# Performance work log

Measured on AMD Instinct MI355X. Metric: run time of the kernel, lower is better.

## Reference

```python
import jax, jax.numpy as jnp
import numpy as np

N_NODES = 100000
N_EDGES = 1600000
D = 128
EPS = 0.0  # train_eps=False -> constant


def setup_inputs() -> dict:
    key = jax.random.key(0)
    k = jax.random.split(key, 6)
    s = 1.0 / np.sqrt(D)
    return {
        "X": jax.random.normal(k[0], (N_NODES, D), dtype=jnp.float32),
        "W1": jax.random.normal(k[1], (D, D), dtype=jnp.float32) * s,
        "b1": jnp.zeros((D,), dtype=jnp.float32),
        "W2": jax.random.normal(k[2], (D, D), dtype=jnp.float32) * s,
        "b2": jnp.zeros((D,), dtype=jnp.float32),
        "edge_src": jax.random.randint(k[3], (N_EDGES,), 0, N_NODES, dtype=jnp.int32),
        "edge_dst": jax.random.randint(k[4], (N_EDGES,), 0, N_NODES, dtype=jnp.int32),
    }


def reference(X, W1, b1, W2, b2, edge_src, edge_dst):
    # v2v sum aggregation: agg[i] = sum_{j in N(i)} X[j]
    msgs = X[edge_src]  # (E, D) gather
    agg = jax.ops.segment_sum(msgs, edge_dst, num_segments=N_NODES)  # (N, D)
    h = (1.0 + EPS) * X + agg
    # MLP: Linear -> ReLU -> Linear
    h = jax.nn.relu(h @ W1 + b1)
    out = h @ W2 + b2
    return out
```

## Files before the change

### kernel.cpp

```cpp
#include <hip/hip_runtime.h>
#include <hip/hip_bf16.h>

#define N_NODES 100000
#define N_EDGES 1600000
#define D 128

#define NBINS 196
#define BINSHIFT 9
#define BINCAP 10000
#define EPB 8192

#define PREP_BIN_BLOCKS 196
#define PREP_W_BLOCKS 8
#define PREP_CVT_BLOCKS 3125

typedef __bf16 bf16x8 __attribute__((ext_vector_type(8)));
typedef short short8 __attribute__((ext_vector_type(8)));
typedef float f32x4 __attribute__((ext_vector_type(4)));

__device__ __forceinline__ unsigned short f2bf(float f) {
  union { float f; unsigned u; } c; c.f = f;
  unsigned u = c.u;
  u += 0x7FFFu + ((u >> 16) & 1u);
  return (unsigned short)(u >> 16);
}
__device__ __forceinline__ float bflo(unsigned u) {
  union { unsigned u; float f; } c; c.u = u << 16; return c.f;
}
__device__ __forceinline__ float bfhi(unsigned u) {
  union { unsigned u; float f; } c; c.u = u & 0xFFFF0000u; return c.f;
}

#define PADK 136

__launch_bounds__(512)
__global__ void k_prep(const float* __restrict__ X, unsigned short* __restrict__ Xb,
                       const float* __restrict__ W1, const float* __restrict__ W2,
                       unsigned short* __restrict__ Wimg,
                       const int* __restrict__ esrc, const int* __restrict__ edst,
                       int* __restrict__ g_bincnt, unsigned* __restrict__ binbuf) {
  __shared__ int cnt[NBINS];
  __shared__ int base[NBINS];
  const int b = blockIdx.x, t = threadIdx.x;

  if (b < PREP_BIN_BLOCKS) {
    const int e0 = b * EPB;
    const int ne = min(EPB, N_EDGES - e0);
    for (int i = t; i < NBINS; i += 512) cnt[i] = 0;
    __syncthreads();
    for (int i = t; i < ne; i += 512)
      atomicAdd(&cnt[edst[e0 + i] >> BINSHIFT], 1);
    __syncthreads();
    for (int i = t; i < NBINS; i += 512) {
      base[i] = atomicAdd(&g_bincnt[i], cnt[i]);
      cnt[i] = 0;
    }
    __syncthreads();
    for (int i = t; i < ne; i += 512) {
      int d = edst[e0 + i];
      int s = esrc[e0 + i];
      int bi = d >> BINSHIFT;
      int pos = base[bi] + atomicAdd(&cnt[bi], 1);
      binbuf[(size_t)bi * BINCAP + pos] = ((unsigned)(d & 511) << 17) | (unsigned)s;
    }
    return;
  }
  if (b < PREP_BIN_BLOCKS + PREP_W_BLOCKS) {
    int bb = b - PREP_BIN_BLOCKS;
    const float* W = (bb & 4) ? W2 : W1;
    unsigned short* img = Wimg + ((bb & 4) ? 128 * PADK : 0);
    int k0 = (bb & 3) * 32;
#pragma unroll
    for (int it = 0; it < 8; ++it) {
      int idx = it * 512 + t;
      int k = k0 + (idx >> 7), n = idx & 127;
      img[n * PADK + k] = f2bf(W[k * 128 + n]);
    }
    return;
  }
  size_t i = ((size_t)(b - PREP_BIN_BLOCKS - PREP_W_BLOCKS) * 512 + t) * 8;
  const float4* p = (const float4*)(X + i);
  float4 a = p[0], c = p[1];
  short8 s;
  s[0] = f2bf(a.x); s[1] = f2bf(a.y); s[2] = f2bf(a.z); s[3] = f2bf(a.w);
  s[4] = f2bf(c.x); s[5] = f2bf(c.y); s[6] = f2bf(c.z); s[7] = f2bf(c.w);
  *(short8*)(Xb + i) = s;
}

__launch_bounds__(512)
__global__ void k_binsort(const unsigned* __restrict__ binbuf, const int* __restrict__ g_bincnt,
                          int* __restrict__ srt, int* __restrict__ deg,
                          int* __restrict__ offs) {
  __shared__ int hist[512];
  __shared__ int scan[512];
  __shared__ int sb[256];
  const int b = blockIdx.x, t = threadIdx.x;

  if (t < 256) sb[t] = (t < NBINS) ? g_bincnt[t] : 0;
  __syncthreads();
  for (int d = 1; d < 256; d <<= 1) {
    int x = 0;
    if (t < 256 && t >= d) x = sb[t - d];
    __syncthreads();
    if (t < 256) sb[t] += x;
    __syncthreads();
  }
  const int cntb = g_bincnt[b];
  const int gbase = (b == 0) ? 0 : sb[b - 1];
  const int n0 = b << BINSHIFT;
  const unsigned* ebuf = binbuf + (size_t)b * BINCAP;

  hist[t] = 0;
  __syncthreads();
  for (int i = t; i < cntb; i += 512)
    atomicAdd(&hist[ebuf[i] >> 17], 1);
  __syncthreads();
  int v = hist[t];
  scan[t] = v;
  __syncthreads();
  for (int d = 1; d < 512; d <<= 1) {
    int x = (t >= d) ? scan[t - d] : 0;
    __syncthreads();
    scan[t] += x;
    __syncthreads();
  }
  int n = n0 + t;
  if (n < N_NODES) {
    deg[n] = v;
    offs[n] = gbase + scan[t] - v;
  }
  hist[t] = scan[t] - v;
  __syncthreads();
  for (int i = t; i < cntb; i += 512) {
    unsigned e = ebuf[i];
    int pos = atomicAdd(&hist[e >> 17], 1);
    srt[gbase + pos] = (int)(e & 0x1FFFFu);
  }
}


__global__ void k_hist(const int* __restrict__ dst, int* __restrict__ deg) {
  int i = blockIdx.x * 256 + threadIdx.x;
  if (i < N_EDGES) atomicAdd(&deg[dst[i]], 1);
}

__global__ void k_scan1(const int* __restrict__ deg, int* __restrict__ offs,
                        int* __restrict__ bsum) {
  __shared__ int s[1024];
  int t = threadIdx.x;
  int i = blockIdx.x * 1024 + t;
  int v = (i < N_NODES) ? deg[i] : 0;
  s[t] = v;
  __syncthreads();
  for (int d = 1; d < 1024; d <<= 1) {
    int x = (t >= d) ? s[t - d] : 0;
    __syncthreads();
    s[t] += x;
    __syncthreads();
  }
  if (i < N_NODES) offs[i] = s[t] - v;
  if (t == 1023) bsum[blockIdx.x] = s[t];
}

__global__ void k_scan2(int* __restrict__ bsum) {
  __shared__ int s[128];
  int t = threadIdx.x;
  int v = (t < 98) ? bsum[t] : 0;
  s[t] = v;
  __syncthreads();
  for (int d = 1; d < 128; d <<= 1) {
    int x = (t >= d) ? s[t - d] : 0;
    __syncthreads();
    s[t] += x;
    __syncthreads();
  }
  if (t < 98) bsum[t] = s[t] - v;
}

__global__ void k_scan3(int* __restrict__ offs, const int* __restrict__ bsum) {
  int i = blockIdx.x * 1024 + threadIdx.x;
  if (i < N_NODES) offs[i] += bsum[blockIdx.x];
}

__global__ void k_bucket(const int* __restrict__ src, const int* __restrict__ dst,
                         int* __restrict__ offs, int* __restrict__ srt) {
  int i = blockIdx.x * 256 + threadIdx.x;
  if (i < N_EDGES) {
    int pos = atomicAdd(&offs[dst[i]], 1);
    srt[pos] = src[i];
  }
}

__global__ void k_gather_bf(const unsigned int* __restrict__ X1,
                            const int* __restrict__ deg, const int* __restrict__ offs,
                            const int* __restrict__ srt, unsigned int* __restrict__ h0) {
  int node = blockIdx.x * 4 + (threadIdx.x >> 6);
  int lane = threadIdx.x & 63;
  unsigned u = X1[(size_t)node * 64 + lane];
  float hx = bflo(u), hy = bfhi(u);
  int e = offs[node];
  int end = e + deg[node];
  for (; e + 8 <= end; e += 8) {
    int s0 = srt[e],     s1 = srt[e + 1], s2 = srt[e + 2], s3 = srt[e + 3];
    int s4 = srt[e + 4], s5 = srt[e + 5], s6 = srt[e + 6], s7 = srt[e + 7];
    unsigned u0 = X1[(size_t)s0 * 64 + lane];
    unsigned u1 = X1[(size_t)s1 * 64 + lane];
    unsigned u2 = X1[(size_t)s2 * 64 + lane];
    unsigned u3 = X1[(size_t)s3 * 64 + lane];
    unsigned u4 = X1[(size_t)s4 * 64 + lane];
    unsigned u5 = X1[(size_t)s5 * 64 + lane];
    unsigned u6 = X1[(size_t)s6 * 64 + lane];
    unsigned u7 = X1[(size_t)s7 * 64 + lane];
    hx += bflo(u0); hy += bfhi(u0);
    hx += bflo(u1); hy += bfhi(u1);
    hx += bflo(u2); hy += bfhi(u2);
    hx += bflo(u3); hy += bfhi(u3);
    hx += bflo(u4); hy += bfhi(u4);
    hx += bflo(u5); hy += bfhi(u5);
    hx += bflo(u6); hy += bfhi(u6);
    hx += bflo(u7); hy += bfhi(u7);
  }
  for (; e + 2 <= end; e += 2) {
    unsigned u0 = X1[(size_t)srt[e] * 64 + lane];
    unsigned u1 = X1[(size_t)srt[e + 1] * 64 + lane];
    hx += bflo(u0); hy += bfhi(u0);
    hx += bflo(u1); hy += bfhi(u1);
  }
  for (; e < end; ++e) {
    unsigned u0 = X1[(size_t)srt[e] * 64 + lane];
    hx += bflo(u0); hy += bfhi(u0);
  }
  h0[(size_t)node * 64 + lane] = ((unsigned)f2bf(hy) << 16) | f2bf(hx);
}

__global__ void k_gather(const float* __restrict__ X, const int* __restrict__ deg,
                         const int* __restrict__ offs, const int* __restrict__ srt,
                         float* __restrict__ out) {
  int node = blockIdx.x * 4 + (threadIdx.x >> 6);
  int lane = threadIdx.x & 63;
  const float2* X2 = (const float2*)X;
  float2 h = X2[(size_t)node * 64 + lane];
  int end = offs[node];
  int dg = deg[node];
  for (int e = end - dg; e < end; ++e) {
    int s = srt[e];
    float2 x = X2[(size_t)s * 64 + lane];
    h.x += x.x; h.y += x.y;
  }
  ((float2*)out)[(size_t)node * 64 + lane] = h;
}

#define BR 256

template <bool BF>
__launch_bounds__(512, 1)
__global__ void k_mlp(const void* __restrict__ h0v,
                      const float* __restrict__ W1, const float* __restrict__ b1,
                      const float* __restrict__ W2, const float* __restrict__ b2,
                      const unsigned short* __restrict__ Wimg,
                      float* __restrict__ out) {
  __shared__ __attribute__((aligned(16))) unsigned short lW[2 * 128 * PADK];
  __shared__ __attribute__((aligned(16))) unsigned short lH[BR * PADK];

  const int t = threadIdx.x;
  const int wave = t >> 6, lane = t & 63;
  const int lr = lane & 15, lg = lane >> 4;
  const int row0 = blockIdx.x * BR;
  const int wrow = row0 + wave * 32;

  if constexpr (BF) {
    const uint4* wi = (const uint4*)Wimg;
    for (int i = t; i < (2 * 128 * PADK * 2) / 16; i += 512)
      ((uint4*)lW)[i] = wi[i];
  } else {
    for (int i = t; i < 128 * 128; i += 512) {
      int k = i >> 7, n = i & 127;
      lW[n * PADK + k] = f2bf(W1[i]);
      lW[128 * PADK + n * PADK + k] = f2bf(W2[i]);
    }
  }

  bf16x8 a[2][4];
#pragma unroll
  for (int tr = 0; tr < 2; ++tr) {
#pragma unroll
    for (int kb = 0; kb < 4; ++kb) {
      int r = wrow + tr * 16 + lr;
      if (r >= N_NODES) r = N_NODES - 1;
      if constexpr (BF) {
        const unsigned short* h0 = (const unsigned short*)h0v;
        a[tr][kb] = __builtin_bit_cast(bf16x8,
            *(const short8*)(h0 + (size_t)r * D + kb * 32 + lg * 8));
      } else {
        const float* h0 = (const float*)h0v;
        const float4* p = (const float4*)(h0 + (size_t)r * D + kb * 32 + lg * 8);
        float4 f0 = p[0], f1 = p[1];
        short8 s;
        s[0] = f2bf(f0.x); s[1] = f2bf(f0.y); s[2] = f2bf(f0.z); s[3] = f2bf(f0.w);
        s[4] = f2bf(f1.x); s[5] = f2bf(f1.y); s[6] = f2bf(f1.z); s[7] = f2bf(f1.w);
        a[tr][kb] = __builtin_bit_cast(bf16x8, s);
      }
    }
  }

  f32x4 acc[2][8];
#pragma unroll
  for (int nc = 0; nc < 8; ++nc) {
    float bb = b1[nc * 16 + lr];
#pragma unroll
    for (int tr = 0; tr < 2; ++tr) acc[tr][nc] = (f32x4){bb, bb, bb, bb};
  }

  __syncthreads();

#pragma unroll
  for (int nc = 0; nc < 8; ++nc) {
#pragma unroll
    for (int kb = 0; kb < 4; ++kb) {
      bf16x8 b = *(const bf16x8*)&lW[(nc * 16 + lr) * PADK + kb * 32 + lg * 8];
#pragma unroll
      for (int tr = 0; tr < 2; ++tr)
        acc[tr][nc] = __builtin_amdgcn_mfma_f32_16x16x32_bf16(a[tr][kb], b, acc[tr][nc], 0, 0, 0);
    }
  }

#pragma unroll
  for (int tr = 0; tr < 2; ++tr) {
#pragma unroll
    for (int nc = 0; nc < 8; ++nc) {
#pragma unroll
      for (int r = 0; r < 4; ++r) {
        float v = acc[tr][nc][r];
        v = v > 0.f ? v : 0.f;
        int lrow = wave * 32 + tr * 16 + lg * 4 + r;
        lH[lrow * PADK + nc * 16 + lr] = f2bf(v);
      }
    }
  }

  __syncthreads();

  bf16x8 a2[2][4];
#pragma unroll
  for (int tr = 0; tr < 2; ++tr) {
#pragma unroll
    for (int kb = 0; kb < 4; ++kb)
      a2[tr][kb] = *(const bf16x8*)&lH[(wave * 32 + tr * 16 + lr) * PADK + kb * 32 + lg * 8];
  }

#pragma unroll
  for (int nc = 0; nc < 8; ++nc) {
    float bb = b2[nc * 16 + lr];
#pragma unroll
    for (int tr = 0; tr < 2; ++tr) acc[tr][nc] = (f32x4){bb, bb, bb, bb};
  }

#pragma unroll
  for (int nc = 0; nc < 8; ++nc) {
#pragma unroll
    for (int kb = 0; kb < 4; ++kb) {
      bf16x8 b = *(const bf16x8*)&lW[128 * PADK + (nc * 16 + lr) * PADK + kb * 32 + lg * 8];
#pragma unroll
      for (int tr = 0; tr < 2; ++tr)
        acc[tr][nc] = __builtin_amdgcn_mfma_f32_16x16x32_bf16(a2[tr][kb], b, acc[tr][nc], 0, 0, 0);
    }
  }

#pragma unroll
  for (int tr = 0; tr < 2; ++tr) {
#pragma unroll
    for (int nc = 0; nc < 8; ++nc) {
#pragma unroll
      for (int r = 0; r < 4; ++r) {
        int row = wrow + tr * 16 + lg * 4 + r;
        if (row < N_NODES) out[(size_t)row * D + nc * 16 + lr] = acc[tr][nc][r];
      }
    }
  }
}

extern "C" void kernel_launch(void* const* d_in, const int* in_sizes, int n_in,
                              void* d_out, int out_size, void* d_ws, size_t ws_size,
                              hipStream_t stream) {
  const float* X  = (const float*)d_in[0];
  const float* W1 = (const float*)d_in[1];
  const float* b1 = (const float*)d_in[2];
  const float* W2 = (const float*)d_in[3];
  const float* b2 = (const float*)d_in[4];
  const int* esrc = (const int*)d_in[5];
  const int* edst = (const int*)d_in[6];
  float* out = (float*)d_out;

  char* ws = (char*)d_ws;
  int* deg      = (int*)(ws);
  int* offs     = (int*)(ws + 400000);
  int* g_bincnt = (int*)(ws + 800000);
  int* srt      = (int*)(ws + 802048);
  unsigned short* Xb  = (unsigned short*)(ws + 7202048);
  unsigned short* h0b = (unsigned short*)(ws + 32802048);
  unsigned* binbuf = (unsigned*)(ws + 32802048);
  unsigned short* Wimg = (unsigned short*)(ws + 58402048);
  const size_t NEED = 58471680;

  if (ws_size >= NEED) {
    hipMemsetAsync(g_bincnt, 0, NBINS * sizeof(int), stream);
    k_prep<<<PREP_BIN_BLOCKS + PREP_W_BLOCKS + PREP_CVT_BLOCKS, 512, 0, stream>>>(
        X, Xb, W1, W2, Wimg, esrc, edst, g_bincnt, binbuf);
    k_binsort<<<NBINS, 512, 0, stream>>>(binbuf, g_bincnt, srt, deg, offs);
    k_gather_bf<<<N_NODES / 4, 256, 0, stream>>>((const unsigned*)Xb, deg, offs, srt,
                                                 (unsigned*)h0b);
    k_mlp<true><<<(N_NODES + BR - 1) / BR, 512, 0, stream>>>(h0b, W1, b1, W2, b2, Wimg, out);
  } else {
    int* bsum = g_bincnt;
    hipMemsetAsync(deg, 0, N_NODES * sizeof(int), stream);
    k_hist  <<<N_EDGES / 256, 256, 0, stream>>>(edst, deg);
    k_scan1 <<<98, 1024, 0, stream>>>(deg, offs, bsum);
    k_scan2 <<<1, 128, 0, stream>>>(bsum);
    k_scan3 <<<98, 1024, 0, stream>>>(offs, bsum);
    k_bucket<<<N_EDGES / 256, 256, 0, stream>>>(esrc, edst, offs, srt);
    k_gather<<<N_NODES / 4, 256, 0, stream>>>(X, deg, offs, srt, out);
    k_mlp<false><<<(N_NODES + BR - 1) / BR, 512, 0, stream>>>(out, W1, b1, W2, b2, nullptr, out);
  }
}
```

Baseline: 135.0 us.

## Fuse neighbor gather into the MLP kernel through shared-memory tiles

```diff
diff --git a/kernel.cpp b/kernel.cpp
--- a/kernel.cpp
+++ b/kernel.cpp
@@ -138,6 +138,133 @@
   }
 }
 
+__launch_bounds__(512, 4)
+__global__ void k_gmlp(const unsigned* __restrict__ X1,
+                       const int* __restrict__ deg, const int* __restrict__ offs,
+                       const int* __restrict__ srt,
+                       const unsigned short* __restrict__ Wimg,
+                       const float* __restrict__ b1v, const float* __restrict__ b2v,
+                       float* __restrict__ out) {
+  __shared__ __attribute__((aligned(16))) unsigned short lW1[128 * PADK];
+  __shared__ __attribute__((aligned(16))) unsigned short lH[128 * PADK];
+
+  const int t = threadIdx.x;
+  const int wave = t >> 6, lane = t & 63;
+  const int row0 = blockIdx.x * 128;
+
+  {
+    const uint4* wi = (const uint4*)Wimg;
+    uint4* lw = (uint4*)lW1;
+    for (int i = t; i < (128 * PADK * 2) / 16; i += 512) lw[i] = wi[i];
+  }
+
+  for (int j = 0; j < 16; ++j) {
+    int lrow = wave * 16 + j;
+    int node = row0 + lrow;
+    unsigned pack = 0;
+    if (node < N_NODES) {
+      unsigned u = X1[(size_t)node * 64 + lane];
+      float hx = bflo(u), hy = bfhi(u);
+      int e = offs[node];
+      int end = e + deg[node];
+      for (; e + 8 <= end; e += 8) {
+        int s0 = srt[e],     s1 = srt[e + 1], s2 = srt[e + 2], s3 = srt[e + 3];
+        int s4 = srt[e + 4], s5 = srt[e + 5], s6 = srt[e + 6], s7 = srt[e + 7];
+        unsigned u0 = X1[(size_t)s0 * 64 + lane];
+        unsigned u1 = X1[(size_t)s1 * 64 + lane];
+        unsigned u2 = X1[(size_t)s2 * 64 + lane];
+        unsigned u3 = X1[(size_t)s3 * 64 + lane];
+        unsigned u4 = X1[(size_t)s4 * 64 + lane];
+        unsigned u5 = X1[(size_t)s5 * 64 + lane];
+        unsigned u6 = X1[(size_t)s6 * 64 + lane];
+        unsigned u7 = X1[(size_t)s7 * 64 + lane];
+        hx += bflo(u0); hy += bfhi(u0);
+        hx += bflo(u1); hy += bfhi(u1);
+        hx += bflo(u2); hy += bfhi(u2);
+        hx += bflo(u3); hy += bfhi(u3);
+        hx += bflo(u4); hy += bfhi(u4);
+        hx += bflo(u5); hy += bfhi(u5);
+        hx += bflo(u6); hy += bfhi(u6);
+        hx += bflo(u7); hy += bfhi(u7);
+      }
+      for (; e + 2 <= end; e += 2) {
+        unsigned u0 = X1[(size_t)srt[e] * 64 + lane];
+        unsigned u1 = X1[(size_t)srt[e + 1] * 64 + lane];
+        hx += bflo(u0); hy += bfhi(u0);
+        hx += bflo(u1); hy += bfhi(u1);
+      }
+      for (; e < end; ++e) {
+        unsigned u0 = X1[(size_t)srt[e] * 64 + lane];
+        hx += bflo(u0); hy += bfhi(u0);
+      }
+      pack = ((unsigned)f2bf(hy) << 16) | f2bf(hx);
+    }
+    *(unsigned*)&lH[lrow * PADK + lane * 2] = pack;
+  }
+
+  __syncthreads();
+
+  const int lr = lane & 15, lg = lane >> 4;
+  bf16x8 a[4];
+#pragma unroll
+  for (int kb = 0; kb < 4; ++kb)
+    a[kb] = *(const bf16x8*)&lH[(wave * 16 + lr) * PADK + kb * 32 + lg * 8];
+
+  f32x4 acc[8];
+#pragma unroll
+  for (int nc = 0; nc < 8; ++nc) {
+    float bb = b1v[nc * 16 + lr];
+    acc[nc] = (f32x4){bb, bb, bb, bb};
+  }
+#pragma unroll
+  for (int nc = 0; nc < 8; ++nc) {
+#pragma unroll
+    for (int kb = 0; kb < 4; ++kb) {
+      bf16x8 b = *(const bf16x8*)&lW1[(nc * 16 + lr) * PADK + kb * 32 + lg * 8];
+      acc[nc] = __builtin_amdgcn_mfma_f32_16x16x32_bf16(a[kb], b, acc[nc], 0, 0, 0);
+    }
+  }
+
+#pragma unroll
+  for (int nc = 0; nc < 8; ++nc) {
+#pragma unroll
+    for (int r = 0; r < 4; ++r) {
+      float v = acc[nc][r];
+      v = v > 0.f ? v : 0.f;
+      lH[(wave * 16 + lg * 4 + r) * PADK + nc * 16 + lr] = f2bf(v);
+    }
+  }
+
+  bf16x8 a2[4];
+#pragma unroll
+  for (int kb = 0; kb < 4; ++kb)
+    a2[kb] = *(const bf16x8*)&lH[(wave * 16 + lr) * PADK + kb * 32 + lg * 8];
+
+#pragma unroll
+  for (int nc = 0; nc < 8; ++nc) {
+    float bb = b2v[nc * 16 + lr];
+    acc[nc] = (f32x4){bb, bb, bb, bb};
+  }
+  const unsigned short* W2i = Wimg + 128 * PADK;
+#pragma unroll
+  for (int nc = 0; nc < 8; ++nc) {
+#pragma unroll
+    for (int kb = 0; kb < 4; ++kb) {
+      bf16x8 b = *(const bf16x8*)&W2i[(nc * 16 + lr) * PADK + kb * 32 + lg * 8];
+      acc[nc] = __builtin_amdgcn_mfma_f32_16x16x32_bf16(a2[kb], b, acc[nc], 0, 0, 0);
+    }
+  }
+
+#pragma unroll
+  for (int nc = 0; nc < 8; ++nc) {
+#pragma unroll
+    for (int r = 0; r < 4; ++r) {
+      int row = row0 + wave * 16 + lg * 4 + r;
+      if (row < N_NODES) out[(size_t)row * D + nc * 16 + lr] = acc[nc][r];
+    }
+  }
+}
+
 
 __global__ void k_hist(const int* __restrict__ dst, int* __restrict__ deg) {
   int i = blockIdx.x * 256 + threadIdx.x;
@@ -189,48 +316,6 @@
     int pos = atomicAdd(&offs[dst[i]], 1);
     srt[pos] = src[i];
   }
-}
-
-__global__ void k_gather_bf(const unsigned int* __restrict__ X1,
-                            const int* __restrict__ deg, const int* __restrict__ offs,
-                            const int* __restrict__ srt, unsigned int* __restrict__ h0) {
-  int node = blockIdx.x * 4 + (threadIdx.x >> 6);
-  int lane = threadIdx.x & 63;
-  unsigned u = X1[(size_t)node * 64 + lane];
-  float hx = bflo(u), hy = bfhi(u);
-  int e = offs[node];
-  int end = e + deg[node];
-  for (; e + 8 <= end; e += 8) {
-    int s0 = srt[e],     s1 = srt[e + 1], s2 = srt[e + 2], s3 = srt[e + 3];
-    int s4 = srt[e + 4], s5 = srt[e + 5], s6 = srt[e + 6], s7 = srt[e + 7];
-    unsigned u0 = X1[(size_t)s0 * 64 + lane];
-    unsigned u1 = X1[(size_t)s1 * 64 + lane];
-    unsigned u2 = X1[(size_t)s2 * 64 + lane];
-    unsigned u3 = X1[(size_t)s3 * 64 + lane];
-    unsigned u4 = X1[(size_t)s4 * 64 + lane];
-    unsigned u5 = X1[(size_t)s5 * 64 + lane];
-    unsigned u6 = X1[(size_t)s6 * 64 + lane];
-    unsigned u7 = X1[(size_t)s7 * 64 + lane];
-    hx += bflo(u0); hy += bfhi(u0);
-    hx += bflo(u1); hy += bfhi(u1);
-    hx += bflo(u2); hy += bfhi(u2);
-    hx += bflo(u3); hy += bfhi(u3);
-    hx += bflo(u4); hy += bfhi(u4);
-    hx += bflo(u5); hy += bfhi(u5);
-    hx += bflo(u6); hy += bfhi(u6);
-    hx += bflo(u7); hy += bfhi(u7);
-  }
-  for (; e + 2 <= end; e += 2) {
-    unsigned u0 = X1[(size_t)srt[e] * 64 + lane];
-    unsigned u1 = X1[(size_t)srt[e + 1] * 64 + lane];
-    hx += bflo(u0); hy += bfhi(u0);
-    hx += bflo(u1); hy += bfhi(u1);
-  }
-  for (; e < end; ++e) {
-    unsigned u0 = X1[(size_t)srt[e] * 64 + lane];
-    hx += bflo(u0); hy += bfhi(u0);
-  }
-  h0[(size_t)node * 64 + lane] = ((unsigned)f2bf(hy) << 16) | f2bf(hx);
 }
 
 __global__ void k_gather(const float* __restrict__ X, const int* __restrict__ deg,
@@ -252,12 +337,10 @@
 
 #define BR 256
 
-template <bool BF>
 __launch_bounds__(512, 1)
-__global__ void k_mlp(const void* __restrict__ h0v,
+__global__ void k_mlp(const float* __restrict__ h0,
                       const float* __restrict__ W1, const float* __restrict__ b1,
                       const float* __restrict__ W2, const float* __restrict__ b2,
-                      const unsigned short* __restrict__ Wimg,
                       float* __restrict__ out) {
   __shared__ __attribute__((aligned(16))) unsigned short lW[2 * 128 * PADK];
   __shared__ __attribute__((aligned(16))) unsigned short lH[BR * PADK];
@@ -268,16 +351,10 @@
   const int row0 = blockIdx.x * BR;
   const int wrow = row0 + wave * 32;
 
-  if constexpr (BF) {
-    const uint4* wi = (const uint4*)Wimg;
-    for (int i = t; i < (2 * 128 * PADK * 2) / 16; i += 512)
-      ((uint4*)lW)[i] = wi[i];
-  } else {
-    for (int i = t; i < 128 * 128; i += 512) {
-      int k = i >> 7, n = i & 127;
-      lW[n * PADK + k] = f2bf(W1[i]);
-      lW[128 * PADK + n * PADK + k] = f2bf(W2[i]);
-    }
+  for (int i = t; i < 128 * 128; i += 512) {
+    int k = i >> 7, n = i & 127;
+    lW[n * PADK + k] = f2bf(W1[i]);
+    lW[128 * PADK + n * PADK + k] = f2bf(W2[i]);
   }
 
   bf16x8 a[2][4];
@@ -287,19 +364,12 @@
     for (int kb = 0; kb < 4; ++kb) {
       int r = wrow + tr * 16 + lr;
       if (r >= N_NODES) r = N_NODES - 1;
-      if constexpr (BF) {
-        const unsigned short* h0 = (const unsigned short*)h0v;
-        a[tr][kb] = __builtin_bit_cast(bf16x8,
-            *(const short8*)(h0 + (size_t)r * D + kb * 32 + lg * 8));
-      } else {
-        const float* h0 = (const float*)h0v;
-        const float4* p = (const float4*)(h0 + (size_t)r * D + kb * 32 + lg * 8);
-        float4 f0 = p[0], f1 = p[1];
-        short8 s;
-        s[0] = f2bf(f0.x); s[1] = f2bf(f0.y); s[2] = f2bf(f0.z); s[3] = f2bf(f0.w);
-        s[4] = f2bf(f1.x); s[5] = f2bf(f1.y); s[6] = f2bf(f1.z); s[7] = f2bf(f1.w);
-        a[tr][kb] = __builtin_bit_cast(bf16x8, s);
-      }
+      const float4* p = (const float4*)(h0 + (size_t)r * D + kb * 32 + lg * 8);
+      float4 f0 = p[0], f1 = p[1];
+      short8 s;
+      s[0] = f2bf(f0.x); s[1] = f2bf(f0.y); s[2] = f2bf(f0.z); s[3] = f2bf(f0.w);
+      s[4] = f2bf(f1.x); s[5] = f2bf(f1.y); s[6] = f2bf(f1.z); s[7] = f2bf(f1.w);
+      a[tr][kb] = __builtin_bit_cast(bf16x8, s);
     }
   }
 
@@ -397,7 +467,6 @@
   int* g_bincnt = (int*)(ws + 800000);
   int* srt      = (int*)(ws + 802048);
   unsigned short* Xb  = (unsigned short*)(ws + 7202048);
-  unsigned short* h0b = (unsigned short*)(ws + 32802048);
   unsigned* binbuf = (unsigned*)(ws + 32802048);
   unsigned short* Wimg = (unsigned short*)(ws + 58402048);
   const size_t NEED = 58471680;
@@ -407,9 +476,8 @@
     k_prep<<<PREP_BIN_BLOCKS + PREP_W_BLOCKS + PREP_CVT_BLOCKS, 512, 0, stream>>>(
         X, Xb, W1, W2, Wimg, esrc, edst, g_bincnt, binbuf);
     k_binsort<<<NBINS, 512, 0, stream>>>(binbuf, g_bincnt, srt, deg, offs);
-    k_gather_bf<<<N_NODES / 4, 256, 0, stream>>>((const unsigned*)Xb, deg, offs, srt,
-                                                 (unsigned*)h0b);
-    k_mlp<true><<<(N_NODES + BR - 1) / BR, 512, 0, stream>>>(h0b, W1, b1, W2, b2, Wimg, out);
+    k_gmlp<<<(N_NODES + 127) / 128, 512, 0, stream>>>((const unsigned*)Xb, deg, offs, srt,
+                                                      Wimg, b1, b2, out);
   } else {
     int* bsum = g_bincnt;
     hipMemsetAsync(deg, 0, N_NODES * sizeof(int), stream);
@@ -419,6 +487,6 @@
     k_scan3 <<<98, 1024, 0, stream>>>(offs, bsum);
     k_bucket<<<N_EDGES / 256, 256, 0, stream>>>(esrc, edst, offs, srt);
     k_gather<<<N_NODES / 4, 256, 0, stream>>>(X, deg, offs, srt, out);
-    k_mlp<false><<<(N_NODES + BR - 1) / BR, 512, 0, stream>>>(out, W1, b1, W2, b2, nullptr, out);
-  }
-}
+    k_mlp   <<<(N_NODES + BR - 1) / BR, 512, 0, stream>>>(out, W1, b1, W2, b2, out);
+  }
+}
```

After: 172.6 us. 27.9% more time.
